# Kernel optimization log

Measured on AMD Instinct MI355X. Metric: run time of the kernel, lower is better.

Reference implementation:

```python
import jax, jax.numpy as jnp
import numpy as np

H = 512
TAU = 5
B = 16384
EPS = 1e-5


def layer_norm(x, gamma, beta):
    mu = jnp.mean(x, axis=-1, keepdims=True)
    var = jnp.var(x, axis=-1, keepdims=True)
    return (x - mu) * jax.lax.rsqrt(var + EPS) * gamma + beta


def setup_inputs() -> dict:
    key = jax.random.key(0)
    ks = jax.random.split(key, 12)
    s = 1.0 / np.sqrt(H)
    inp = {
        "T_t": jax.random.normal(ks[0], (B, H), jnp.float32),
        "S_t": jax.random.normal(ks[1], (B, H), jnp.float32),
        "t_att": jax.random.normal(ks[2], (TAU, B, H), jnp.float32),
        "s_att": jax.random.normal(ks[3], (TAU, B, H), jnp.float32),
        # Lin_t_next: in_features(H) -> H, + LayerNorm
        "W_tn": jax.random.uniform(ks[4], (H, H), jnp.float32, -s, s),
        "b_tn": jnp.zeros((H,), jnp.float32),
        "g_tn": jnp.ones((H,), jnp.float32),
        "be_tn": jnp.zeros((H,), jnp.float32),
        # Lin_s_next: H -> H, + LayerNorm
        "W_sn": jax.random.uniform(ks[5], (H, H), jnp.float32, -s, s),
        "b_sn": jnp.zeros((H,), jnp.float32),
        "g_sn": jnp.ones((H,), jnp.float32),
        "be_sn": jnp.zeros((H,), jnp.float32),
        # Lin_t: H -> 3H, + LayerNorm
        "W_t": jax.random.uniform(ks[6], (H, 3 * H), jnp.float32, -s, s),
        "b_t": jnp.zeros((3 * H,), jnp.float32),
        "g_t": jnp.ones((3 * H,), jnp.float32),
        "be_t": jnp.zeros((3 * H,), jnp.float32),
        # Lin_s: H -> 3H, + LayerNorm
        "W_s": jax.random.uniform(ks[7], (H, 3 * H), jnp.float32, -s, s),
        "b_s": jnp.zeros((3 * H,), jnp.float32),
        "g_s": jnp.ones((3 * H,), jnp.float32),
        "be_s": jnp.zeros((3 * H,), jnp.float32),
    }
    return inp


def reference(T_t, S_t, t_att, s_att,
              W_tn, b_tn, g_tn, be_tn,
              W_sn, b_sn, g_sn, be_sn,
              W_t, b_t, g_t, be_t,
              W_s, b_s, g_s, be_s):
    s_next = layer_norm(S_t @ W_sn + b_sn, g_sn, be_sn)        # [B,H]
    t_next = layer_norm(T_t @ W_tn + b_tn, g_tn, be_tn)        # [B,H]

    # attention weights over tau trend steps
    scale = 1.0 / jnp.sqrt(jnp.asarray(H, T_t.dtype))
    weights = jnp.einsum('tbh,bh->tb', s_att, s_next) * scale   # [tau,B]
    weights = jax.nn.softmax(weights, axis=0)[..., None]        # [tau,B,1]
    T_trend = jnp.sum(t_att * weights, axis=0)                  # [B,H]

    t_att_gate = jax.nn.sigmoid(t_next)
    T_fusion = T_t * t_att_gate + (1.0 - t_att_gate) * T_trend

    T_concat = layer_norm(T_fusion @ W_t + b_t, g_t, be_t)      # [B,3H]
    S_concat = layer_norm(S_t @ W_s + b_s, g_s, be_s)           # [B,3H]
    t_g, t_t, t_s = jnp.split(T_concat, 3, axis=1)
    s_g, s_t, s_s = jnp.split(S_concat, 3, axis=1)

    T_gate = jax.nn.sigmoid(t_g)
    S_gate = jax.nn.sigmoid(s_g)
    T_new = T_gate * t_t + (1.0 - T_gate) * s_t
    S_new = S_gate * s_s + (1.0 - S_gate) * t_s
    S_new = S_new + S_t  # cell_mode == 'residual'
    return (T_new, S_new)
```

## Files before the change

kernel.cpp:

```cpp
#include <hip/hip_runtime.h>

#define Bsz 16384
#define Hd  512
#define TAUn 5
#define EPSv 1e-5f

typedef short bf16x8 __attribute__((ext_vector_type(8)));
typedef float f32x4  __attribute__((ext_vector_type(4)));

__device__ __forceinline__ float bf2f(short s) {
    union { unsigned u; float f; } v;
    v.u = ((unsigned)(unsigned short)s) << 16;
    return v.f;
}
__device__ __forceinline__ short f2bf(float f) {
    union { float f; unsigned u; } v; v.f = f;
    unsigned r = v.u + 0x7fffu + ((v.u >> 16) & 1u);
    return (short)(r >> 16);
}
__device__ __forceinline__ float sigm(float x) {
    return 1.0f / (1.0f + expf(-x));
}

__device__ __forceinline__ void gload16(const void* gsrc, void* lds) {
    __builtin_amdgcn_global_load_lds(
        (const __attribute__((address_space(1))) void*)gsrc,
        (__attribute__((address_space(3))) void*)lds, 16, 0, 0);
}

__device__ __forceinline__ float load1(const void* p, size_t i, int isbf) {
    return isbf ? bf2f(((const short*)p)[i]) : ((const float*)p)[i];
}
__device__ __forceinline__ void load8f(const void* p, size_t off, int isbf, float o[8]) {
    if (isbf) {
        bf16x8 v = *(const bf16x8*)((const short*)p + off);
#pragma unroll
        for (int j = 0; j < 8; ++j) o[j] = bf2f(v[j]);
    } else {
        const float* f = (const float*)p + off;
        float4 a = *(const float4*)f, b = *(const float4*)(f + 4);
        o[0]=a.x; o[1]=a.y; o[2]=a.z; o[3]=a.w; o[4]=b.x; o[5]=b.y; o[6]=b.z; o[7]=b.w;
    }
}
__device__ __forceinline__ bf16x8 load8bf(const void* p, size_t off, int isbf) {
    if (isbf) return *(const bf16x8*)((const short*)p + off);
    const float* f = (const float*)p + off;
    bf16x8 r;
#pragma unroll
    for (int j = 0; j < 8; ++j) r[j] = f2bf(f[j]);
    return r;
}

__global__ void detect_dtype(const void* g_tn, int* flag) {
    if (threadIdx.x == 0 && blockIdx.x == 0)
        *flag = (((const unsigned*)g_tn)[0] == 0x3F803F80u) ? 1 : 0;
}

__global__ void transpose_any(const void* __restrict__ in, short* __restrict__ out,
                              int K, int N, const int* __restrict__ flagp) {
    __shared__ short tile[32][33];
    const int isbf = *flagp;
    int n0 = blockIdx.x * 32, k0 = blockIdx.y * 32;
    int tx = threadIdx.x, ty = threadIdx.y;
    for (int i = ty; i < 32; i += 8) {
        size_t idx = (size_t)(k0 + i) * N + n0 + tx;
        tile[i][tx] = isbf ? ((const short*)in)[idx] : f2bf(((const float*)in)[idx]);
    }
    __syncthreads();
    for (int i = ty; i < 32; i += 8)
        out[(size_t)(n0 + i) * K + k0 + tx] = tile[tx][i];
}

__global__ __launch_bounds__(256) void conv_bf16(const void* __restrict__ in,
                                                 short* __restrict__ out,
                                                 const int* __restrict__ flagp) {
    const int isbf = *flagp;
    size_t i = ((size_t)blockIdx.x * 256 + threadIdx.x) * 8;
    *(bf16x8*)(out + i) = load8bf(in, i, isbf);
}

__global__ __launch_bounds__(256) void pack_weights(const void* __restrict__ in,
                                                    short* __restrict__ out,
                                                    int N, const int* __restrict__ flagp) {
    const int isbf = *flagp;
    const int lane = threadIdx.x & 63;
    const int packet = blockIdx.x * 4 + (threadIdx.x >> 6);
    const int nc = packet >> 4;
    const int kc = packet & 15;
    const int n  = nc * 16 + (lane & 15);
    const int kb = kc * 32 + (lane >> 4) * 8;
    bf16x8 v;
#pragma unroll
    for (int j = 0; j < 8; ++j) {
        size_t idx = (size_t)(kb + j) * N + n;
        v[j] = isbf ? ((const short*)in)[idx] : f2bf(((const float*)in)[idx]);
    }
    *(bf16x8*)(out + (size_t)packet * 512 + lane * 8) = v;
}

__global__ __launch_bounds__(256) void gemm128(
    const short* __restrict__ A, const short* __restrict__ BT,
    short* __restrict__ C, int N)
{
    __shared__ short As[2][128 * 32];
    __shared__ short Bs[2][128 * 32];
    const int tid  = threadIdx.x;
    const int wv   = tid >> 6, lane = tid & 63;
    const int m16  = lane & 15, quad = lane >> 4;
    const int mt = blockIdx.x & 127, nt = blockIdx.x >> 7;
    const int m0 = mt * 128, n0 = nt * 128;
    const int wm = wv >> 1, wn = wv & 1;

    f32x4 acc[16];
#pragma unroll
    for (int i = 0; i < 16; ++i) acc[i] = (f32x4){0.f, 0.f, 0.f, 0.f};

    auto STAGE = [&](int buf, int kc) {
        const int k0 = kc * 32;
#pragma unroll
        for (int o = 0; o < 2; ++o) {
            int g = o * 256 + tid;
            int row = g >> 2, unit = g & 3;
            gload16(A  + (size_t)(m0 + row) * Hd + k0 + unit * 8,
                    (short*)As[buf] + (size_t)(o * 256 + wv * 64) * 8);
            gload16(BT + (size_t)(n0 + row) * Hd + k0 + unit * 8,
                    (short*)Bs[buf] + (size_t)(o * 256 + wv * 64) * 8);
        }
    };

    STAGE(0, 0);
    __syncthreads();
    for (int kc = 0; kc < 16; ++kc) {
        const int cur = kc & 1;
        if (kc < 15) STAGE(cur ^ 1, kc + 1);
        bf16x8 a[4], b[4];
#pragma unroll
        for (int f = 0; f < 4; ++f) {
            a[f] = *(const bf16x8*)&As[cur][(wm * 64 + f * 16 + m16) * 32 + quad * 8];
            b[f] = *(const bf16x8*)&Bs[cur][(wn * 64 + f * 16 + m16) * 32 + quad * 8];
        }
#pragma unroll
        for (int fm = 0; fm < 4; ++fm)
#pragma unroll
            for (int fn = 0; fn < 4; ++fn)
                acc[fm * 4 + fn] = __builtin_amdgcn_mfma_f32_16x16x32_bf16(
                    a[fm], b[fn], acc[fm * 4 + fn], 0, 0, 0);
        __syncthreads();
    }

#pragma unroll
    for (int fm = 0; fm < 4; ++fm)
#pragma unroll
        for (int fn = 0; fn < 4; ++fn) {
            int col = n0 + wn * 64 + fn * 16 + m16;
#pragma unroll
            for (int r = 0; r < 4; ++r) {
                int row = m0 + wm * 64 + fm * 16 + quad * 4 + r;
                C[(size_t)row * N + col] = f2bf(acc[fm * 4 + fn][r]);
            }
        }
}

__global__ __launch_bounds__(256) void kernelA2(
    const short* __restrict__ Cs, const short* __restrict__ Ct,
    const void* __restrict__ T_t, const void* __restrict__ t_att, const void* __restrict__ s_att,
    const void* __restrict__ b_tn, const void* __restrict__ g_tn, const void* __restrict__ be_tn,
    const void* __restrict__ b_sn, const void* __restrict__ g_sn, const void* __restrict__ be_sn,
    short* __restrict__ T_fus, const int* __restrict__ flagp)
{
    const int isbf = *flagp;
    const int lane = threadIdx.x & 63;
    const size_t row = (size_t)blockIdx.x * 4 + (threadIdx.x >> 6);
    const int c0 = lane * 8;
    const float hinv = 1.0f / 512.0f;

    bf16x8 cs8 = *(const bf16x8*)(Cs + row * Hd + c0);
    bf16x8 ct8 = *(const bf16x8*)(Ct + row * Hd + c0);
    float bs[8], btn[8];
    load8f(b_sn, c0, isbf, bs);
    load8f(b_tn, c0, isbf, btn);
    float xs[8], xt[8];
    float s1 = 0, s2 = 0, t1 = 0, t2 = 0;
#pragma unroll
    for (int j = 0; j < 8; ++j) {
        float x = bf2f(cs8[j]) + bs[j];
        float y = bf2f(ct8[j]) + btn[j];
        xs[j] = x; xt[j] = y;
        s1 += x; s2 += x * x; t1 += y; t2 += y * y;
    }
    for (int mk = 32; mk >= 1; mk >>= 1) {
        s1 += __shfl_xor(s1, mk); s2 += __shfl_xor(s2, mk);
        t1 += __shfl_xor(t1, mk); t2 += __shfl_xor(t2, mk);
    }
    float muS = s1 * hinv, rS = rsqrtf(s2 * hinv - muS * muS + EPSv);
    float muT = t1 * hinv, rT = rsqrtf(t2 * hinv - muT * muT + EPSv);

    float gs[8], bes[8], gtv[8], bet[8];
    load8f(g_sn,  c0, isbf, gs);
    load8f(be_sn, c0, isbf, bes);
    load8f(g_tn,  c0, isbf, gtv);
    load8f(be_tn, c0, isbf, bet);
#pragma unroll
    for (int j = 0; j < 8; ++j) {
        xs[j] = (xs[j] - muS) * rS * gs[j] + bes[j];
        xt[j] = (xt[j] - muT) * rT * gtv[j] + bet[j];
    }

    const float scale = 0.044194173824159216f;
    float w[TAUn];
    for (int t = 0; t < TAUn; ++t) {
        float sa[8];
        load8f(s_att, ((size_t)t * Bsz + row) * Hd + c0, isbf, sa);
        float p = 0;
#pragma unroll
        for (int j = 0; j < 8; ++j) p += sa[j] * xs[j];
        for (int mk = 32; mk >= 1; mk >>= 1) p += __shfl_xor(p, mk);
        w[t] = p * scale;
    }
    float mx = -1e30f;
    for (int t = 0; t < TAUn; ++t) mx = fmaxf(mx, w[t]);
    float ssum = 0;
    for (int t = 0; t < TAUn; ++t) { w[t] = expf(w[t] - mx); ssum += w[t]; }
    float sinv = 1.0f / ssum;
    for (int t = 0; t < TAUn; ++t) w[t] *= sinv;

    float tt[8];
    load8f(T_t, row * Hd + c0, isbf, tt);
    float trend[8] = {0, 0, 0, 0, 0, 0, 0, 0};
    for (int t = 0; t < TAUn; ++t) {
        float ta[8];
        load8f(t_att, ((size_t)t * Bsz + row) * Hd + c0, isbf, ta);
#pragma unroll
        for (int j = 0; j < 8; ++j) trend[j] += w[t] * ta[j];
    }
    bf16x8 o;
#pragma unroll
    for (int j = 0; j < 8; ++j) {
        float g = sigm(xt[j]);
        o[j] = f2bf(tt[j] * g + (1.f - g) * trend[j]);
    }
    *(bf16x8*)(T_fus + row * Hd + c0) = o;
}

__global__ __launch_bounds__(256) void kernelC2(
    const short* __restrict__ Cu, const short* __restrict__ Cv, const void* __restrict__ S_t,
    const void* __restrict__ b_t, const void* __restrict__ g_t, const void* __restrict__ be_t,
    const void* __restrict__ b_s, const void* __restrict__ g_s, const void* __restrict__ be_s,
    void* __restrict__ out, const int* __restrict__ flagp)
{
    const int isbf = *flagp;
    const int lane = threadIdx.x & 63;
    const size_t row = (size_t)blockIdx.x * 4 + (threadIdx.x >> 6);
    const float n3inv = 1.0f / 1536.0f;

    float u[3][8], v[3][8];
    float su = 0, qu = 0, sv = 0, qv = 0;
#pragma unroll
    for (int k = 0; k < 3; ++k) {
        int c0 = (k * 64 + lane) * 8;
        bf16x8 a = *(const bf16x8*)(Cu + row * 1536 + c0);
        bf16x8 b = *(const bf16x8*)(Cv + row * 1536 + c0);
        float bt[8], bs[8];
        load8f(b_t, c0, isbf, bt);
        load8f(b_s, c0, isbf, bs);
#pragma unroll
        for (int j = 0; j < 8; ++j) {
            float x = bf2f(a[j]) + bt[j];
            float y = bf2f(b[j]) + bs[j];
            u[k][j] = x; v[k][j] = y;
            su += x; qu += x * x; sv += y; qv += y * y;
        }
    }
    for (int mk = 32; mk >= 1; mk >>= 1) {
        su += __shfl_xor(su, mk); qu += __shfl_xor(qu, mk);
        sv += __shfl_xor(sv, mk); qv += __shfl_xor(qv, mk);
    }
    float muU = su * n3inv, rU = rsqrtf(qu * n3inv - muU * muU + EPSv);
    float muV = sv * n3inv, rV = rsqrtf(qv * n3inv - muV * muV + EPSv);

    float guv[3][8], beu[3][8], gvv[3][8], bev[3][8];
#pragma unroll
    for (int k = 0; k < 3; ++k) {
        int c0 = (k * 64 + lane) * 8;
        load8f(g_t,  c0, isbf, guv[k]);
        load8f(be_t, c0, isbf, beu[k]);
        load8f(g_s,  c0, isbf, gvv[k]);
        load8f(be_s, c0, isbf, bev[k]);
    }
    float stv[8];
    load8f(S_t, row * Hd + lane * 8, isbf, stv);

    float Tn[8], Sn[8];
#pragma unroll
    for (int j = 0; j < 8; ++j) {
        float ug = (u[0][j] - muU) * rU * guv[0][j] + beu[0][j];
        float ut = (u[1][j] - muU) * rU * guv[1][j] + beu[1][j];
        float us = (u[2][j] - muU) * rU * guv[2][j] + beu[2][j];
        float vg = (v[0][j] - muV) * rV * gvv[0][j] + bev[0][j];
        float vt = (v[1][j] - muV) * rV * gvv[1][j] + bev[1][j];
        float vs = (v[2][j] - muV) * rV * gvv[2][j] + bev[2][j];
        float Tg = sigm(ug), Sg = sigm(vg);
        Tn[j] = Tg * ut + (1.f - Tg) * vt;
        Sn[j] = Sg * vs + (1.f - Sg) * us + stv[j];
    }

    size_t o0 = row * Hd + lane * 8;
    size_t o1 = (size_t)Bsz * Hd + o0;
    if (isbf) {
        bf16x8 oT, oS;
#pragma unroll
        for (int j = 0; j < 8; ++j) { oT[j] = f2bf(Tn[j]); oS[j] = f2bf(Sn[j]); }
        *(bf16x8*)((short*)out + o0) = oT;
        *(bf16x8*)((short*)out + o1) = oS;
    } else {
        float* of = (float*)out;
        *(float4*)(of + o0)     = (float4){Tn[0], Tn[1], Tn[2], Tn[3]};
        *(float4*)(of + o0 + 4) = (float4){Tn[4], Tn[5], Tn[6], Tn[7]};
        *(float4*)(of + o1)     = (float4){Sn[0], Sn[1], Sn[2], Sn[3]};
        *(float4*)(of + o1 + 4) = (float4){Sn[4], Sn[5], Sn[6], Sn[7]};
    }
}

__global__ __launch_bounds__(256) void kernelA(
    const void* __restrict__ T_t, const void* __restrict__ S_t,
    const void* __restrict__ t_att, const void* __restrict__ s_att,
    const short* __restrict__ WtnP, const short* __restrict__ WsnP,
    const void* __restrict__ b_tn, const void* __restrict__ g_tn, const void* __restrict__ be_tn,
    const void* __restrict__ b_sn, const void* __restrict__ g_sn, const void* __restrict__ be_sn,
    short* __restrict__ T_fus, const int* __restrict__ flagp)
{
    __shared__ float xs[16][Hd + 4];
    __shared__ float xt[16][Hd + 4];
    __shared__ float red[4][16][16];
    __shared__ float stat[4][16];
    __shared__ float wts[TAUn][16];

    const int isbf = *flagp;
    const int tid  = threadIdx.x;
    const int wave = tid >> 6;
    const int lane = tid & 63;
    const int m16  = lane & 15;
    const int quad = lane >> 4;
    const int row0 = blockIdx.x * 16;

    f32x4 accS[8], accT[8];
#pragma unroll
    for (int i = 0; i < 8; ++i) { accS[i] = (f32x4){0.f,0.f,0.f,0.f}; accT[i] = (f32x4){0.f,0.f,0.f,0.f}; }

    const size_t arow = (size_t)(row0 + m16) * Hd + quad * 8;
    const int nw = wave * 128;

    for (int kc = 0; kc < 16; ++kc) {
        const int k0 = kc * 32;
        bf16x8 aS = load8bf(S_t, arow + k0, isbf);
        bf16x8 aT = load8bf(T_t, arow + k0, isbf);
#pragma unroll
        for (int t = 0; t < 8; ++t) {
            size_t off = (size_t)((((wave * 8 + t) * 16 + kc) * 64) + lane) * 8;
            bf16x8 bS = *(const bf16x8*)(WsnP + off);
            bf16x8 bT = *(const bf16x8*)(WtnP + off);
            accS[t] = __builtin_amdgcn_mfma_f32_16x16x32_bf16(aS, bS, accS[t], 0, 0, 0);
            accT[t] = __builtin_amdgcn_mfma_f32_16x16x32_bf16(aT, bT, accT[t], 0, 0, 0);
        }
    }
#pragma unroll
    for (int t = 0; t < 8; ++t) {
        int col = nw + t * 16 + m16;
        float bs = load1(b_sn, col, isbf), bt = load1(b_tn, col, isbf);
#pragma unroll
        for (int r = 0; r < 4; ++r) {
            xs[quad * 4 + r][col] = accS[t][r] + bs;
            xt[quad * 4 + r][col] = accT[t][r] + bt;
        }
    }
    __syncthreads();

    {
        int r = tid >> 4, lw = tid & 15;
        float s1 = 0, s2 = 0, t1 = 0, t2 = 0;
        for (int c = lw; c < Hd; c += 16) {
            float v = xs[r][c]; s1 += v; s2 += v * v;
            float u = xt[r][c]; t1 += u; t2 += u * u;
        }
        red[0][r][lw] = s1; red[1][r][lw] = s2; red[2][r][lw] = t1; red[3][r][lw] = t2;
    }
    __syncthreads();
    if (tid < 16) {
        float a = 0, b = 0, c = 0, d = 0;
        for (int i = 0; i < 16; ++i) { a += red[0][tid][i]; b += red[1][tid][i]; c += red[2][tid][i]; d += red[3][tid][i]; }
        float muS = a / Hd, varS = b / Hd - muS * muS;
        float muT = c / Hd, varT = d / Hd - muT * muT;
        stat[0][tid] = muS; stat[1][tid] = rsqrtf(varS + EPSv);
        stat[2][tid] = muT; stat[3][tid] = rsqrtf(varT + EPSv);
    }
    __syncthreads();
    for (int idx = tid; idx < 16 * Hd; idx += 256) {
        int r = idx >> 9, c = idx & (Hd - 1);
        xs[r][c] = (xs[r][c] - stat[0][r]) * stat[1][r] * load1(g_sn, c, isbf) + load1(be_sn, c, isbf);
        xt[r][c] = (xt[r][c] - stat[2][r]) * stat[3][r] * load1(g_tn, c, isbf) + load1(be_tn, c, isbf);
    }
    __syncthreads();

    const float scale = 0.044194173824159216f;
    for (int r2 = 0; r2 < 4; ++r2) {
        int row = wave * 4 + r2;
        size_t b = (size_t)(row0 + row);
        float xsv[8];
#pragma unroll
        for (int j = 0; j < 8; ++j) xsv[j] = xs[row][lane * 8 + j];
        for (int t = 0; t < TAUn; ++t) {
            float sa[8];
            load8f(s_att, ((size_t)t * Bsz + b) * Hd + lane * 8, isbf, sa);
            float p = 0;
#pragma unroll
            for (int j = 0; j < 8; ++j) p += sa[j] * xsv[j];
            for (int off = 32; off > 0; off >>= 1) p += __shfl_xor(p, off);
            if (lane == 0) wts[t][row] = p * scale;
        }
    }
    __syncthreads();
    if (tid < 16) {
        float mx = -1e30f;
        for (int t = 0; t < TAUn; ++t) mx = fmaxf(mx, wts[t][tid]);
        float e[TAUn], s = 0;
        for (int t = 0; t < TAUn; ++t) { e[t] = expf(wts[t][tid] - mx); s += e[t]; }
        for (int t = 0; t < TAUn; ++t) wts[t][tid] = e[t] / s;
    }
    __syncthreads();

    for (int it = 0; it < 4; ++it) {
        int c = tid + it * 256;
        int row = c >> 6, h0 = (c & 63) * 8;
        size_t b = (size_t)(row0 + row);
        float tt[8];
        load8f(T_t, b * Hd + h0, isbf, tt);
        float w[TAUn];
        for (int t = 0; t < TAUn; ++t) w[t] = wts[t][row];
        float ta[TAUn][8];
        for (int t = 0; t < TAUn; ++t)
            load8f(t_att, ((size_t)t * Bsz + b) * Hd + h0, isbf, ta[t]);
        bf16x8 o;
#pragma unroll
        for (int j = 0; j < 8; ++j) {
            float g = sigm(xt[row][h0 + j]);
            float trend = 0;
            for (int t = 0; t < TAUn; ++t) trend += w[t] * ta[t][j];
            o[j] = f2bf(tt[j] * g + (1.f - g) * trend);
        }
        *(bf16x8*)(T_fus + b * Hd + h0) = o;
    }
}

__global__ __launch_bounds__(512) void kernelB(
    const short* __restrict__ T_fus, const void* __restrict__ S_t,
    const short* __restrict__ WtP, const short* __restrict__ WsP,
    const void* __restrict__ b_t, const void* __restrict__ g_t, const void* __restrict__ be_t,
    const void* __restrict__ b_s, const void* __restrict__ g_s, const void* __restrict__ be_s,
    void* __restrict__ out, const int* __restrict__ flagp)
{
    __shared__ float red[4][16][8];
    __shared__ float stat[4][16];

    const int isbf = *flagp;
    const int tid  = threadIdx.x;
    const int wave = tid >> 6;
    const int lane = tid & 63;
    const int m16  = lane & 15;
    const int quad = lane >> 4;
    const int row0 = blockIdx.x * 16;
    const int N3 = 3 * Hd;

    f32x4 accU[12], accV[12];
#pragma unroll
    for (int i = 0; i < 12; ++i) { accU[i] = (f32x4){0.f,0.f,0.f,0.f}; accV[i] = (f32x4){0.f,0.f,0.f,0.f}; }

    const short* A1 = T_fus + (size_t)(row0 + m16) * Hd + quad * 8;
    const size_t a2row = (size_t)(row0 + m16) * Hd + quad * 8;

    for (int kc = 0; kc < 16; ++kc) {
        const int k0 = kc * 32;
        bf16x8 a1 = *(const bf16x8*)(A1 + k0);
        bf16x8 a2 = load8bf(S_t, a2row + k0, isbf);
#pragma unroll
        for (int th = 0; th < 3; ++th) {
#pragma unroll
            for (int t = 0; t < 4; ++t) {
                int nc = th * 32 + wave * 4 + t;
                size_t off = (size_t)(((nc * 16 + kc) * 64) + lane) * 8;
                bf16x8 bU = *(const bf16x8*)(WtP + off);
                bf16x8 bV = *(const bf16x8*)(WsP + off);
                accU[th * 4 + t] = __builtin_amdgcn_mfma_f32_16x16x32_bf16(a1, bU, accU[th * 4 + t], 0, 0, 0);
                accV[th * 4 + t] = __builtin_amdgcn_mfma_f32_16x16x32_bf16(a2, bV, accV[th * 4 + t], 0, 0, 0);
            }
        }
    }
#pragma unroll
    for (int i = 0; i < 12; ++i) {
        int th = i >> 2, t = i & 3;
        int col = th * Hd + wave * 64 + t * 16 + m16;
        float bu = load1(b_t, col, isbf), bv = load1(b_s, col, isbf);
#pragma unroll
        for (int r = 0; r < 4; ++r) { accU[i][r] += bu; accV[i][r] += bv; }
    }
    float sU[4] = {0,0,0,0}, qU[4] = {0,0,0,0}, sV[4] = {0,0,0,0}, qV[4] = {0,0,0,0};
#pragma unroll
    for (int i = 0; i < 12; ++i)
#pragma unroll
        for (int r = 0; r < 4; ++r) {
            float u = accU[i][r]; sU[r] += u; qU[r] += u * u;
            float v = accV[i][r]; sV[r] += v; qV[r] += v * v;
        }
    for (int mk = 8; mk >= 1; mk >>= 1)
#pragma unroll
        for (int r = 0; r < 4; ++r) {
            sU[r] += __shfl_xor(sU[r], mk); qU[r] += __shfl_xor(qU[r], mk);
            sV[r] += __shfl_xor(sV[r], mk); qV[r] += __shfl_xor(qV[r], mk);
        }
    if (m16 == 0)
#pragma unroll
        for (int r = 0; r < 4; ++r) {
            int row = quad * 4 + r;
            red[0][row][wave] = sU[r]; red[1][row][wave] = qU[r];
            red[2][row][wave] = sV[r]; red[3][row][wave] = qV[r];
        }
    __syncthreads();
    if (tid < 16) {
        float a = 0, b = 0, c = 0, d = 0;
        for (int w = 0; w < 8; ++w) { a += red[0][tid][w]; b += red[1][tid][w]; c += red[2][tid][w]; d += red[3][tid][w]; }
        float muU = a / N3, varU = b / N3 - muU * muU;
        float muV = c / N3, varV = d / N3 - muV * muV;
        stat[0][tid] = muU; stat[1][tid] = rsqrtf(varU + EPSv);
        stat[2][tid] = muV; stat[3][tid] = rsqrtf(varV + EPSv);
    }
    __syncthreads();

    short* out_b = (short*)out;
    float* out_f = (float*)out;
#pragma unroll
    for (int t = 0; t < 4; ++t) {
        int c = wave * 64 + t * 16 + m16;
        float gt0 = load1(g_t, c, isbf),        bt0 = load1(be_t, c, isbf);
        float gt1 = load1(g_t, c + 512, isbf),  bt1 = load1(be_t, c + 512, isbf);
        float gt2 = load1(g_t, c + 1024, isbf), bt2 = load1(be_t, c + 1024, isbf);
        float gs0 = load1(g_s, c, isbf),        bs0 = load1(be_s, c, isbf);
        float gs1 = load1(g_s, c + 512, isbf),  bs1 = load1(be_s, c + 512, isbf);
        float gs2 = load1(g_s, c + 1024, isbf), bs2 = load1(be_s, c + 1024, isbf);
#pragma unroll
        for (int r = 0; r < 4; ++r) {
            int row = quad * 4 + r;
            size_t grow = (size_t)(row0 + row);
            float mU = stat[0][row], rU = stat[1][row];
            float mV = stat[2][row], rV = stat[3][row];
            float ug = (accU[t][r]     - mU) * rU * gt0 + bt0;
            float ut = (accU[4 + t][r] - mU) * rU * gt1 + bt1;
            float us = (accU[8 + t][r] - mU) * rU * gt2 + bt2;
            float vg = (accV[t][r]     - mV) * rV * gs0 + bs0;
            float vt = (accV[4 + t][r] - mV) * rV * gs1 + bs1;
            float vs = (accV[8 + t][r] - mV) * rV * gs2 + bs2;
            float Tg = sigm(ug), Sg = sigm(vg);
            float Tn = Tg * ut + (1.f - Tg) * vt;
            float Sn = Sg * vs + (1.f - Sg) * us + load1(S_t, grow * Hd + c, isbf);
            size_t i0 = grow * Hd + c;
            size_t i1 = (size_t)Bsz * Hd + grow * Hd + c;
            if (isbf) { out_b[i0] = f2bf(Tn); out_b[i1] = f2bf(Sn); }
            else      { out_f[i0] = Tn;       out_f[i1] = Sn; }
        }
    }
}

extern "C" void kernel_launch(void* const* d_in, const int* in_sizes, int n_in,
                              void* d_out, int out_size, void* d_ws, size_t ws_size,
                              hipStream_t stream) {
    const void* T_t   = d_in[0];
    const void* S_t   = d_in[1];
    const void* t_att = d_in[2];
    const void* s_att = d_in[3];
    const void* W_tn  = d_in[4];
    const void* b_tn  = d_in[5];
    const void* g_tn  = d_in[6];
    const void* be_tn = d_in[7];
    const void* W_sn  = d_in[8];
    const void* b_sn  = d_in[9];
    const void* g_sn  = d_in[10];
    const void* be_sn = d_in[11];
    const void* W_t   = d_in[12];
    const void* b_t   = d_in[13];
    const void* g_t   = d_in[14];
    const void* be_t  = d_in[15];
    const void* W_s   = d_in[16];
    const void* b_s   = d_in[17];
    const void* g_s   = d_in[18];
    const void* be_s  = d_in[19];

    int*   flag = (int*)d_ws;
    short* p    = (short*)d_ws + 8;
    short* WtnP = p; p += 512 * 512;
    short* WsnP = p; p += 512 * 512;
    short* Tfus = p; p += (size_t)Bsz * 512;
    short* WtP  = p; p += (size_t)512 * 1536;
    short* WsP  = p; p += (size_t)512 * 1536;
    short* WtnT = p; p += 512 * 512;
    short* WsnT = p; p += 512 * 512;
    short* WtT  = p; p += (size_t)512 * 1536;
    short* WsT  = p; p += (size_t)512 * 1536;
    short* S_bf = p; p += (size_t)Bsz * 512;
    short* T_bf = p; p += (size_t)Bsz * 512;
    short* Cu   = p; p += (size_t)Bsz * 1536;
    short* Cv   = p; p += (size_t)Bsz * 1536;
    size_t need = (size_t)((char*)p - (char*)d_ws);

    detect_dtype<<<1, 64, 0, stream>>>(g_tn, flag);
    dim3 tb(32, 8);

    if (ws_size >= need) {
        transpose_any<<<dim3(16, 16), tb, 0, stream>>>(W_tn, WtnT, 512, 512, flag);
        transpose_any<<<dim3(16, 16), tb, 0, stream>>>(W_sn, WsnT, 512, 512, flag);
        transpose_any<<<dim3(48, 16), tb, 0, stream>>>(W_t,  WtT,  512, 1536, flag);
        transpose_any<<<dim3(48, 16), tb, 0, stream>>>(W_s,  WsT,  512, 1536, flag);

        const int bf_host = (in_sizes && in_sizes[0] == (int)((size_t)Bsz * Hd * 2)) ? 1 : 0;
        const short* As = bf_host ? (const short*)S_t : S_bf;
        const short* At = bf_host ? (const short*)T_t : T_bf;
        if (!bf_host) {
            conv_bf16<<<4096, 256, 0, stream>>>(S_t, S_bf, flag);
            conv_bf16<<<4096, 256, 0, stream>>>(T_t, T_bf, flag);
        }

        gemm128<<<4 * 128, 256, 0, stream>>>(As, WsnT, Cu, 512);
        gemm128<<<4 * 128, 256, 0, stream>>>(At, WtnT, Cv, 512);
        kernelA2<<<Bsz / 4, 256, 0, stream>>>(Cu, Cv, T_t, t_att, s_att,
                                              b_tn, g_tn, be_tn, b_sn, g_sn, be_sn, Tfus, flag);

        gemm128<<<12 * 128, 256, 0, stream>>>(Tfus, WtT, Cu, 1536);
        gemm128<<<12 * 128, 256, 0, stream>>>(As, WsT, Cv, 1536);
        kernelC2<<<Bsz / 4, 256, 0, stream>>>(Cu, Cv, S_t,
                                              b_t, g_t, be_t, b_s, g_s, be_s, d_out, flag);
    } else {
        pack_weights<<<dim3((32 * 16) / 4), 256, 0, stream>>>(W_tn, WtnP, 512, flag);
        pack_weights<<<dim3((32 * 16) / 4), 256, 0, stream>>>(W_sn, WsnP, 512, flag);
        pack_weights<<<dim3((96 * 16) / 4), 256, 0, stream>>>(W_t,  WtP,  1536, flag);
        pack_weights<<<dim3((96 * 16) / 4), 256, 0, stream>>>(W_s,  WsP,  1536, flag);
        kernelA<<<Bsz / 16, 256, 0, stream>>>(T_t, S_t, t_att, s_att, WtnP, WsnP,
                                              b_tn, g_tn, be_tn, b_sn, g_sn, be_sn, Tfus, flag);
        kernelB<<<Bsz / 16, 512, 0, stream>>>(Tfus, S_t, WtP, WsP,
                                              b_t, g_t, be_t, b_s, g_s, be_s, d_out, flag);
    }
}
```

Baseline: 656.0 us.

## Fuse LayerNorm and attention dot reductions into one pass; swizzle GEMM tile order

kernelA2 now issues all s_att and t_att loads up front. It expands the attention dot product algebraically, sum(sa*(x-mu)*r*g+be) = r*(sum(sa*x*g) - mu*sum(sa*g)) + sum(sa*be), so the LayerNorm statistics and all five attention logits come from one batched butterfly reduction instead of six sequential ones. This removes the serialized shuffle chains and exposes more memory-level parallelism, at the cost of more live registers. The GEMM also remaps block indices in groups of eight, which changes the tile order and may improve L2 reuse.

Result: no change. 657.9 us (+0.3%).

```diff
diff --git a/kernel.cpp b/kernel.cpp
--- a/kernel.cpp
+++ b/kernel.cpp
@@ -107,7 +107,11 @@
     const int tid  = threadIdx.x;
     const int wv   = tid >> 6, lane = tid & 63;
     const int m16  = lane & 15, quad = lane >> 4;
-    const int mt = blockIdx.x & 127, nt = blockIdx.x >> 7;
+    const int NT   = N >> 7;
+    const int nwg  = gridDim.x;
+    const int cpx  = nwg >> 3;
+    const int swz  = (blockIdx.x & 7) * cpx + (blockIdx.x >> 3);
+    const int mt = swz / NT, nt = swz % NT;
     const int m0 = mt * 128, n0 = nt * 128;
     const int wm = wv >> 1, wn = wv & 1;
 
@@ -176,68 +180,76 @@
 
     bf16x8 cs8 = *(const bf16x8*)(Cs + row * Hd + c0);
     bf16x8 ct8 = *(const bf16x8*)(Ct + row * Hd + c0);
-    float bs[8], btn[8];
-    load8f(b_sn, c0, isbf, bs);
-    load8f(b_tn, c0, isbf, btn);
-    float xs[8], xt[8];
-    float s1 = 0, s2 = 0, t1 = 0, t2 = 0;
-#pragma unroll
-    for (int j = 0; j < 8; ++j) {
-        float x = bf2f(cs8[j]) + bs[j];
-        float y = bf2f(ct8[j]) + btn[j];
-        xs[j] = x; xt[j] = y;
-        s1 += x; s2 += x * x; t1 += y; t2 += y * y;
-    }
-    for (int mk = 32; mk >= 1; mk >>= 1) {
-        s1 += __shfl_xor(s1, mk); s2 += __shfl_xor(s2, mk);
-        t1 += __shfl_xor(t1, mk); t2 += __shfl_xor(t2, mk);
-    }
-    float muS = s1 * hinv, rS = rsqrtf(s2 * hinv - muS * muS + EPSv);
-    float muT = t1 * hinv, rT = rsqrtf(t2 * hinv - muT * muT + EPSv);
-
-    float gs[8], bes[8], gtv[8], bet[8];
+    float sa[TAUn][8];
+#pragma unroll
+    for (int t = 0; t < TAUn; ++t)
+        load8f(s_att, ((size_t)t * Bsz + row) * Hd + c0, isbf, sa[t]);
+    float bs[8], btn[8], gs[8], bes[8];
+    load8f(b_sn,  c0, isbf, bs);
+    load8f(b_tn,  c0, isbf, btn);
     load8f(g_sn,  c0, isbf, gs);
     load8f(be_sn, c0, isbf, bes);
+
+    float x[8], y[8];
+    float red[4 + 3 * TAUn];
+#pragma unroll
+    for (int i = 0; i < 4 + 3 * TAUn; ++i) red[i] = 0.f;
+#pragma unroll
+    for (int j = 0; j < 8; ++j) {
+        float xv = bf2f(cs8[j]) + bs[j];
+        float yv = bf2f(ct8[j]) + btn[j];
+        x[j] = xv; y[j] = yv;
+        red[0] += xv; red[1] += xv * xv;
+        red[2] += yv; red[3] += yv * yv;
+        float xg = xv * gs[j];
+#pragma unroll
+        for (int t = 0; t < TAUn; ++t) {
+            red[4 + t]  += sa[t][j] * xg;
+            red[9 + t]  += sa[t][j] * gs[j];
+            red[14 + t] += sa[t][j] * bes[j];
+        }
+    }
+#pragma unroll
+    for (int mk = 32; mk >= 1; mk >>= 1)
+#pragma unroll
+        for (int i = 0; i < 4 + 3 * TAUn; ++i)
+            red[i] += __shfl_xor(red[i], mk);
+
+    float tt[8];
+    load8f(T_t, row * Hd + c0, isbf, tt);
+    float ta[TAUn][8];
+#pragma unroll
+    for (int t = 0; t < TAUn; ++t)
+        load8f(t_att, ((size_t)t * Bsz + row) * Hd + c0, isbf, ta[t]);
+    float gtv[8], bet[8];
     load8f(g_tn,  c0, isbf, gtv);
     load8f(be_tn, c0, isbf, bet);
-#pragma unroll
-    for (int j = 0; j < 8; ++j) {
-        xs[j] = (xs[j] - muS) * rS * gs[j] + bes[j];
-        xt[j] = (xt[j] - muT) * rT * gtv[j] + bet[j];
-    }
+
+    float muS = red[0] * hinv, rS = rsqrtf(red[1] * hinv - muS * muS + EPSv);
+    float muT = red[2] * hinv, rT = rsqrtf(red[3] * hinv - muT * muT + EPSv);
 
     const float scale = 0.044194173824159216f;
     float w[TAUn];
-    for (int t = 0; t < TAUn; ++t) {
-        float sa[8];
-        load8f(s_att, ((size_t)t * Bsz + row) * Hd + c0, isbf, sa);
-        float p = 0;
-#pragma unroll
-        for (int j = 0; j < 8; ++j) p += sa[j] * xs[j];
-        for (int mk = 32; mk >= 1; mk >>= 1) p += __shfl_xor(p, mk);
-        w[t] = p * scale;
-    }
+#pragma unroll
+    for (int t = 0; t < TAUn; ++t)
+        w[t] = (rS * (red[4 + t] - muS * red[9 + t]) + red[14 + t]) * scale;
     float mx = -1e30f;
+#pragma unroll
     for (int t = 0; t < TAUn; ++t) mx = fmaxf(mx, w[t]);
     float ssum = 0;
+#pragma unroll
     for (int t = 0; t < TAUn; ++t) { w[t] = expf(w[t] - mx); ssum += w[t]; }
     float sinv = 1.0f / ssum;
-    for (int t = 0; t < TAUn; ++t) w[t] *= sinv;
-
-    float tt[8];
-    load8f(T_t, row * Hd + c0, isbf, tt);
-    float trend[8] = {0, 0, 0, 0, 0, 0, 0, 0};
-    for (int t = 0; t < TAUn; ++t) {
-        float ta[8];
-        load8f(t_att, ((size_t)t * Bsz + row) * Hd + c0, isbf, ta);
-#pragma unroll
-        for (int j = 0; j < 8; ++j) trend[j] += w[t] * ta[j];
-    }
+
     bf16x8 o;
 #pragma unroll
     for (int j = 0; j < 8; ++j) {
-        float g = sigm(xt[j]);
-        o[j] = f2bf(tt[j] * g + (1.f - g) * trend[j]);
+        float trend = 0;
+#pragma unroll
+        for (int t = 0; t < TAUn; ++t) trend += w[t] * ta[t][j];
+        trend *= sinv;
+        float g = sigm((y[j] - muT) * rT * gtv[j] + bet[j]);
+        o[j] = f2bf(tt[j] * g + (1.f - g) * trend);
     }
     *(bf16x8*)(T_fus + row * Hd + c0) = o;
 }
```
